# Kernel tuning notes

Hardware: AMD Instinct MI355X
Metric: run time of the kernel (lower is better)

## Reference

```python
import jax, jax.numpy as jnp
import numpy as np

N = 8192      # nodes
DIN = 128     # in_channels
DH = 64       # hidden_channels (dim_out, num_heads=1)
DOUT = 32     # out_channels
RATIO = 0.5
K_KEEP = int(np.ceil(RATIO * N))  # SAGPooling keep count (single graph)
LN_EPS = 1e-5


def _linear_params(k, fan_in, fan_out):
    kw, kb = jax.random.split(k)
    W = jax.random.normal(kw, (fan_in, fan_out), dtype=jnp.float32) / jnp.sqrt(jnp.float32(fan_in))
    b = jax.random.normal(kb, (fan_out,), dtype=jnp.float32) * 0.01
    return W, b


def setup_inputs() -> dict:
    key = jax.random.key(0)
    ks = jax.random.split(key, 8)
    x = jax.random.normal(ks[0], (N, DIN), dtype=jnp.float32)
    batch = jnp.zeros((N,), dtype=jnp.int64)  # single graph
    Wq, bq = _linear_params(ks[1], DIN, DH)
    Wk, bk = _linear_params(ks[2], DIN, DH)
    Wv, bv = _linear_params(ks[3], DIN, DH)
    gcn_W, gcn_b = _linear_params(ks[4], DH, DH)       # GCNConv weight/bias
    score_W, score_b = _linear_params(ks[5], DH, 1)    # SAGPooling score GCNConv
    ln_g = jnp.ones((DH,), dtype=jnp.float32)
    ln_b = jnp.zeros((DH,), dtype=jnp.float32)
    head_W, head_b = _linear_params(ks[6], DH, DOUT)
    return dict(x=x, batch=batch, Wq=Wq, bq=bq, Wk=Wk, bk=bk, Wv=Wv, bv=bv,
                gcn_W=gcn_W, gcn_b=gcn_b, score_W=score_W, score_b=score_b,
                ln_g=ln_g, ln_b=ln_b, head_W=head_W, head_b=head_b)


def _forward(x, Wq, bq, Wk, bk, Wv, bv, gcn_W, gcn_b, score_W, score_b,
             ln_g, ln_b, head_W, head_b):
    # --- self-attention over all nodes (num_heads = 1) ---
    Q = x @ Wq + bq                                        # [N, DH]
    K = x @ Wk + bk
    V = x @ Wv + bv
    attn = jax.nn.softmax(Q @ K.T / jnp.sqrt(jnp.float32(DH)), axis=-1)  # [N, N]
    h = attn @ V                                           # [N, DH]

    # --- edge construction: threshold attention, ensure self-loops ---
    # (attn > 0.5).nonzero() -> edge set; empty -> self-loop fallback; then
    # add_self_loops. Dense equivalent: A = max(mask, I).
    eye = jnp.eye(N, dtype=x.dtype)
    A = jnp.maximum((attn > 0.5).astype(x.dtype), eye)     # [N, N], diag = 1

    # symmetric GCN normalization  D^{-1/2} A D^{-1/2}
    dinv = jax.lax.rsqrt(A.sum(axis=1))                    # [N]
    An = dinv[:, None] * A * dinv[None, :]                 # [N, N]

    # --- GCNConv layer ---
    g = An @ (h @ gcn_W) + gcn_b                           # [N, DH]

    # --- SAGPooling: GCNConv scorer -> tanh -> global top-k (single graph) ---
    score = jnp.tanh((An @ (g @ score_W) + score_b).squeeze(-1))  # [N]
    top_scores, perm = jax.lax.top_k(score, K_KEEP)        # sorted desc, like PyG topk
    xp = g[perm] * top_scores[:, None]                     # [K, DH], multiplier = 1

    # --- LayerNorm + ReLU (dropout is identity in eval) ---
    mu = xp.mean(axis=-1, keepdims=True)
    var = xp.var(axis=-1, keepdims=True)
    xp = (xp - mu) * jax.lax.rsqrt(var + LN_EPS) * ln_g + ln_b
    xp = jax.nn.relu(xp)

    # --- prediction head ---
    return xp @ head_W + head_b                            # [K, DOUT]


def reference(x, batch, Wq, bq, Wk, bk, Wv, bv, gcn_W, gcn_b,
              score_W, score_b, ln_g, ln_b, head_W, head_b):
    del batch  # single graph; grouping has no effect on the math
    return _forward(x, Wq, bq, Wk, bk, Wv, bv, gcn_W, gcn_b,
                    score_W, score_b, ln_g, ln_b, head_W, head_b)
```

## Files before the change

kernel.cpp:

```cpp
#include <hip/hip_runtime.h>
#include <hip/hip_bf16.h>
#include <cstdio>

typedef __hip_bfloat16 bf16;
typedef __attribute__((ext_vector_type(8))) short v8s;
typedef __attribute__((ext_vector_type(4))) short v4s;
typedef __attribute__((ext_vector_type(4))) float v4f;
typedef __attribute__((ext_vector_type(4))) double v4d;

#define MFMA16(a, b, c) __builtin_amdgcn_mfma_f32_16x16x32_bf16((a), (b), (c), 0, 0, 0)

#define NN 8192
#define DIN 128
#define DH 64
#define DOUT 32
#define KKEEP 4096
#define SPLITS 16
#define SPATT 8

__device__ __forceinline__ float bf2f(bf16 v) { return __bfloat162float(v); }
__device__ __forceinline__ short f2bfs(float f) {
  __hip_bfloat16 h = __float2bfloat16(f);
  return *reinterpret_cast<short*>(&h);
}
__device__ __forceinline__ bf16 f2bf(float v) { return __float2bfloat16(v); }

__device__ __forceinline__ double exp_d(double s) {
  const double L2E    = 1.4426950408889634074;
  const double LN2_HI = 6.93147180369123816490e-01;
  const double LN2_LO = 1.90821492927058770002e-10;
  double t  = s * L2E;
  double kf = rint(t);
  double r  = fma(-kf, LN2_HI, s);
  r = fma(-kf, LN2_LO, r);
  double p = 1.0 / 362880.0;
  p = fma(p, r, 1.0 / 40320.0);
  p = fma(p, r, 1.0 / 5040.0);
  p = fma(p, r, 1.0 / 720.0);
  p = fma(p, r, 1.0 / 120.0);
  p = fma(p, r, 1.0 / 24.0);
  p = fma(p, r, 1.0 / 6.0);
  p = fma(p, r, 0.5);
  p = fma(p, r, 1.0);
  p = fma(p, r, 1.0);
  int k = (int)kf;
  long long bits = ((long long)(1023 + k)) << 52;
  double sc = __longlong_as_double(bits);
  return p * sc;
}

__global__ void k0_ucb(const float* __restrict__ gW, const float* __restrict__ sW,
                       const float* __restrict__ gb, double* __restrict__ u) {
  int c = threadIdx.x;
  double acc = 0.0, accb = 0.0;
  for (int d = 0; d < DH; ++d) {
    double swd = (double)sW[d];
    acc  = fma((double)gW[c * DH + d], swd, acc);
    accb = fma((double)gb[d], swd, accb);
  }
  u[c] = acc;
  if (c == 0) u[64] = accb;
}

__global__ __launch_bounds__(256) void k1_prep(
    const float* __restrict__ x, const float* __restrict__ Wq, const float* __restrict__ bq,
    const float* __restrict__ Wk, const float* __restrict__ bk, const float* __restrict__ Wv,
    const float* __restrict__ bv, const double* __restrict__ u,
    double* __restrict__ Qd, double* __restrict__ Kd, double* __restrict__ w,
    bf16* __restrict__ Qb, bf16* __restrict__ Kb, bf16* __restrict__ Vt) {
  __shared__ double xs[16][DIN];
  int t = threadIdx.x;
  int nb = blockIdx.x * 16;
  for (int idx = t; idx < 16 * DIN; idx += 256)
    xs[idx >> 7][idx & 127] = (double)x[(size_t)nb * DIN + idx];
  __syncthreads();
  int d = t & 63;
  int sub = t >> 6;
  double bqd = (double)bq[d];
  double bkd = (double)bk[d];
  double bvd = (double)bv[d];
  double ud = u[d];
  for (int pass = 0; pass < 4; ++pass) {
    int n = pass * 4 + sub;
    double aq = bqd, ak = bkd, av = bvd;
#pragma unroll 8
    for (int c = 0; c < DIN; ++c) {
      double xv = xs[n][c];
      aq = fma(xv, (double)Wq[c * DH + d], aq);
      ak = fma(xv, (double)Wk[c * DH + d], ak);
      av = fma(xv, (double)Wv[c * DH + d], av);
    }
    aq *= 0.125;
    int node = nb + n;
    Qd[(size_t)node * DH + d] = aq;
    Kd[(size_t)node * DH + d] = ak;
    Qb[(size_t)node * DH + d] = f2bf((float)aq);
    Kb[(size_t)node * DH + d] = f2bf((float)ak);
    Vt[(size_t)d * NN + node] = f2bf((float)av);
    double pw = av * ud;
#pragma unroll
    for (int off = 32; off; off >>= 1) pw += __shfl_xor(pw, off);
    if (d == 0) w[node] = pw;
  }
}

__global__ __launch_bounds__(256) void k2_scores(
    const double* __restrict__ Qd, const double* __restrict__ Kd, const double* __restrict__ w,
    double* __restrict__ Zp, double* __restrict__ Wp, double* __restrict__ Ep, int* __restrict__ Jp) {
  __shared__ __align__(16) double Kbuf[2][16][66];
  const int t = threadIdx.x;
  const int wv = t >> 6;
  const int l = t & 63;
  const int li = l & 15, lg = l >> 4;
  const int rb = (blockIdx.x & 127) * 64;
  const int sp = blockIdx.x >> 7;
  const int cbeg = sp * (NN / SPLITS);

  double qreg[16];
  const double* qrow = Qd + (size_t)(rb + 16 * wv + li) * DH + lg;
#pragma unroll
  for (int tt = 0; tt < 16; ++tt) qreg[tt] = qrow[4 * tt];

  {
    const double* src = Kd + (size_t)cbeg * DH;
    int r = t >> 4, c = (t & 15) * 4;
    *(double2*)&Kbuf[0][r][c]     = *(const double2*)&src[r * DH + c];
    *(double2*)&Kbuf[0][r][c + 2] = *(const double2*)&src[r * DH + c + 2];
  }
  __syncthreads();

  double Zt[4] = {0, 0, 0, 0}, Wt[4] = {0, 0, 0, 0}, Et[4] = {-1, -1, -1, -1};
  int Jt[4] = {0, 0, 0, 0};

  const int NT = (NN / SPLITS) / 16;
  for (int kt = 0; kt < NT; ++kt) {
    const int buf = kt & 1;
    if (kt + 1 < NT) {
      const double* src = Kd + (size_t)(cbeg + (kt + 1) * 16) * DH;
      int r = t >> 4, c = (t & 15) * 4;
      *(double2*)&Kbuf[buf ^ 1][r][c]     = *(const double2*)&src[r * DH + c];
      *(double2*)&Kbuf[buf ^ 1][r][c + 2] = *(const double2*)&src[r * DH + c + 2];
    }
    v4d acc = (v4d){0.0, 0.0, 0.0, 0.0};
#pragma unroll
    for (int tt = 0; tt < 16; ++tt) {
      double bfrag = Kbuf[buf][li][4 * tt + lg];
      acc = __builtin_amdgcn_mfma_f64_16x16x4f64(qreg[tt], bfrag, acc, 0, 0, 0);
    }
    const int col = cbeg + kt * 16 + li;
    const double wj = w[col];
#pragma unroll
    for (int v = 0; v < 4; ++v) {
      double e = exp_d(acc[v]);
      Zt[v] += e;
      Wt[v] = fma(e, wj, Wt[v]);
      if (e > Et[v]) { Et[v] = e; Jt[v] = col; }
    }
    __syncthreads();
  }

#pragma unroll
  for (int v = 0; v < 4; ++v) {
#pragma unroll
    for (int m = 1; m < 16; m <<= 1) {
      Zt[v] += __shfl_xor(Zt[v], m);
      Wt[v] += __shfl_xor(Wt[v], m);
      double e2 = __shfl_xor(Et[v], m);
      int j2 = __shfl_xor(Jt[v], m);
      if (e2 > Et[v] || (e2 == Et[v] && j2 < Jt[v])) { Et[v] = e2; Jt[v] = j2; }
    }
  }
  if (li == 0) {
#pragma unroll
    for (int v = 0; v < 4; ++v) {
      int row = rb + 16 * wv + lg + 4 * v;
      Zp[sp * NN + row] = Zt[v];
      Wp[sp * NN + row] = Wt[v];
      Ep[sp * NN + row] = Et[v];
      Jp[sp * NN + row] = Jt[v];
    }
  }
}

__global__ void k3_combine(const double* __restrict__ Zp, const double* __restrict__ Wp,
                           const double* __restrict__ Ep, const int* __restrict__ Jp,
                           double* __restrict__ tau, int* __restrict__ extra, int* __restrict__ jmA) {
  int i = blockIdx.x * 256 + threadIdx.x;
  double Z = 0, W = 0, E = -1;
  int J = 0;
  for (int sp = 0; sp < SPLITS; ++sp) {
    Z += Zp[sp * NN + i];
    W += Wp[sp * NN + i];
    double e = Ep[sp * NN + i];
    if (e > E || (e == E && Jp[sp * NN + i] < J)) { E = e; J = Jp[sp * NN + i]; }
  }
  tau[i] = W / Z;
  extra[i] = (E > 0.5 * Z) && (J != i);
  jmA[i] = J & (NN - 1);
}

__global__ __launch_bounds__(256) void k4_mfma(const bf16* __restrict__ Qb, const bf16* __restrict__ Kb,
                                               const bf16* __restrict__ Vt,
                                               float* __restrict__ hp, float* __restrict__ zp) {
  __shared__ __align__(16) short P[4][16 * 40];
  const int t = threadIdx.x;
  const int wv = t >> 6;
  const int l = t & 63, g = l >> 4, li = l & 15;
  const int qb = (blockIdx.x & 127) * 64 + wv * 16;
  const int sp = blockIdx.x >> 7;
  short* Pw = &P[wv][0];
  const v8s q0 = *(const v8s*)(Qb + (size_t)(qb + li) * DH + g * 8);
  const v8s q1 = *(const v8s*)(Qb + (size_t)(qb + li) * DH + 32 + g * 8);
  v4f hacc[4];
#pragma unroll
  for (int db = 0; db < 4; ++db) hacc[db] = (v4f){0.f, 0.f, 0.f, 0.f};
  float zl = 0.f;
  const int kbeg = sp * (NN / SPATT);
  for (int jb = kbeg; jb < kbeg + NN / SPATT; jb += 32) {
    const bf16* kp = Kb + (size_t)(jb + li) * DH + g * 8;
    v8s ka0 = *(const v8s*)(kp);
    v8s ka1 = *(const v8s*)(kp + 32);
    v8s kb0 = *(const v8s*)(kp + 16 * DH);
    v8s kb1 = *(const v8s*)(kp + 16 * DH + 32);
    v4f c0 = (v4f){0.f, 0.f, 0.f, 0.f}, c1 = (v4f){0.f, 0.f, 0.f, 0.f};
    c0 = MFMA16(ka0, q0, c0);
    c0 = MFMA16(ka1, q1, c0);
    c1 = MFMA16(kb0, q0, c1);
    c1 = MFMA16(kb1, q1, c1);
    v4s p0, p1;
#pragma unroll
    for (int r = 0; r < 4; ++r) {
      short b0 = f2bfs(__expf(c0[r]));
      short b1 = f2bfs(__expf(c1[r]));
      p0[r] = b0;
      p1[r] = b1;
      zl += bf2f(*reinterpret_cast<bf16*>(&b0));
      zl += bf2f(*reinterpret_cast<bf16*>(&b1));
    }
    *(v4s*)&Pw[li * 40 + g * 4] = p0;
    *(v4s*)&Pw[li * 40 + 16 + g * 4] = p1;
    v8s pf = *(const v8s*)&Pw[li * 40 + g * 8];
#pragma unroll
    for (int db = 0; db < 4; ++db) {
      const v8s vb = *(const v8s*)(Vt + (size_t)(db * 16 + li) * NN + jb + g * 8);
      hacc[db] = MFMA16(pf, vb, hacc[db]);
    }
  }
  zl += __shfl_xor(zl, 16);
  zl += __shfl_xor(zl, 32);
  if (g == 0) zp[sp * NN + qb + li] = zl;
#pragma unroll
  for (int r = 0; r < 4; ++r) {
    int row = qb + g * 4 + r;
#pragma unroll
    for (int db = 0; db < 4; ++db)
      hp[((size_t)sp * NN + row) * DH + db * 16 + li] = hacc[db][r];
  }
}

__global__ __launch_bounds__(256) void k9_hM(const float* __restrict__ hp, const float* __restrict__ zp,
                                             const float* __restrict__ gW, float* __restrict__ M) {
  __shared__ float xs[4][DH];
  int t = threadIdx.x;
  int sub = t >> 6, d = t & 63;
  int n = blockIdx.x * 4 + sub;
  float Z = 0.f, H = 0.f;
#pragma unroll
  for (int sp = 0; sp < SPATT; ++sp) {
    Z += zp[sp * NN + n];
    H += hp[((size_t)sp * NN + n) * DH + d];
  }
  xs[sub][d] = H / Z;
  __syncthreads();
  float acc = 0.f;
#pragma unroll 8
  for (int c = 0; c < DH; ++c) acc = fmaf(xs[sub][c], gW[c * DH + d], acc);
  M[(size_t)n * DH + d] = acc;
}

__global__ void k5_t(const double* __restrict__ tau, const int* __restrict__ extra,
                     const int* __restrict__ jmA, const double* __restrict__ u, double* __restrict__ tarr) {
  int i = blockIdx.x * 256 + threadIdx.x;
  int ex = extra[i];
  double di = ex ? 0.70710678118654752440 : 1.0;
  double acc = di * tau[i];
  if (ex) {
    int j = jmA[i] & (NN - 1);
    double dj = extra[j] ? 0.70710678118654752440 : 1.0;
    acc = fma(dj, tau[j], acc);
  }
  tarr[i] = fma(di, acc, u[64]);
}

__global__ void k6_pre(const double* __restrict__ tarr, const int* __restrict__ extra,
                       const int* __restrict__ jmA, const float* __restrict__ score_b,
                       double* __restrict__ pre, float* __restrict__ sc32, int* __restrict__ cnt) {
  int i = blockIdx.x * 256 + threadIdx.x;
  int ex = extra[i];
  double di = ex ? 0.70710678118654752440 : 1.0;
  double acc = di * tarr[i];
  if (ex) {
    int j = jmA[i] & (NN - 1);
    double dj = extra[j] ? 0.70710678118654752440 : 1.0;
    acc = fma(dj, tarr[j], acc);
  }
  double p = fma(di, acc, (double)score_b[0]);
  pre[i] = p;
  sc32[i] = (float)tanh(p);
  cnt[i] = 0;
}

__global__ void k7_rank(const double* __restrict__ pre, int* __restrict__ cnt) {
  __shared__ double pj[512];
  int i = (blockIdx.x & 31) * 256 + threadIdx.x;
  int j0 = (blockIdx.x >> 5) * 512;
  for (int k = threadIdx.x; k < 512; k += 256) pj[k] = pre[j0 + k];
  __syncthreads();
  double si = pre[i];
  int c = 0;
#pragma unroll 8
  for (int j = 0; j < 512; ++j) {
    double v = pj[j];
    c += (v > si || (v == si && (j0 + j) < i));
  }
  atomicAdd(&cnt[i], c);
}

__global__ void k8_sel(const int* __restrict__ cnt, int* __restrict__ sel) {
  int i = blockIdx.x * 256 + threadIdx.x;
  unsigned r = (unsigned)cnt[i];
  if (r < KKEEP) sel[r] = i;
}

__global__ __launch_bounds__(256) void k11_head(const float* __restrict__ M, const int* __restrict__ extra,
                                                const int* __restrict__ jmA, const float* __restrict__ gb,
                                                const float* __restrict__ sc32, const int* __restrict__ sel,
                                                const float* __restrict__ lg, const float* __restrict__ lb,
                                                const float* __restrict__ hW, const float* __restrict__ hb,
                                                float* __restrict__ out) {
  __shared__ float xs[4][DH];
  int t = threadIdx.x;
  int wv = t >> 6, d = t & 63;
  int p = blockIdx.x * 4 + wv;
  int i = sel[p] & (NN - 1);
  int ex = extra[i];
  float di = ex ? 0.70710678f : 1.0f;
  float acc0 = di * M[(size_t)i * DH + d];
  if (ex) {
    int j = jmA[i] & (NN - 1);
    acc0 = fmaf(extra[j] ? 0.70710678f : 1.0f, M[(size_t)j * DH + d], acc0);
  }
  float gval = fmaf(di, acc0, gb[d]);
  float v = gval * sc32[i];
  float s1 = v;
#pragma unroll
  for (int off = 32; off; off >>= 1) s1 += __shfl_xor(s1, off);
  float mu = s1 * (1.0f / 64.0f);
  float dv = v - mu;
  float s2 = dv * dv;
#pragma unroll
  for (int off = 32; off; off >>= 1) s2 += __shfl_xor(s2, off);
  float var = s2 * (1.0f / 64.0f);
  float xn = dv * rsqrtf(var + 1e-5f) * lg[d] + lb[d];
  xs[wv][d] = fmaxf(xn, 0.0f);
  __syncthreads();
  if (t < 128) {
    int r = t >> 5, o = t & 31;
    float acc = hb[o];
#pragma unroll 8
    for (int c = 0; c < DH; ++c) acc = fmaf(xs[r][c], hW[c * DOUT + o], acc);
    out[(size_t)(blockIdx.x * 4 + r) * DOUT + o] = acc;
  }
}

#define MB 1048576ull
constexpr size_t OFF_QD   = 0 * MB;
constexpr size_t OFF_KD   = 4 * MB;
constexpr size_t OFF_M    = 16 * MB;
constexpr size_t OFF_ZP   = 20 * MB;
constexpr size_t OFF_WP   = 21 * MB;
constexpr size_t OFF_EP   = 22 * MB;
constexpr size_t OFF_JP   = 23 * MB;
constexpr size_t OFF_W    = 24 * MB;
constexpr size_t OFF_U    = 25 * MB;
constexpr size_t OFF_TAU  = 26 * MB;
constexpr size_t OFF_EX   = 27 * MB;
constexpr size_t OFF_JM   = 28 * MB;
constexpr size_t OFF_T    = 29 * MB;
constexpr size_t OFF_PRE  = 30 * MB;
constexpr size_t OFF_SC   = 31 * MB;
constexpr size_t OFF_CNT  = 32 * MB;
constexpr size_t OFF_SEL  = 33 * MB;
constexpr size_t OFF_HP   = 34 * MB;
constexpr size_t OFF_ZATT = 50 * MB;
constexpr size_t OFF_QB   = 51 * MB;
constexpr size_t OFF_KB   = 52 * MB;
constexpr size_t OFF_VT   = 53 * MB;
constexpr size_t WS_NEEDED = 54 * MB;

extern "C" void kernel_launch(void* const* d_in, const int* in_sizes, int n_in,
                              void* d_out, int out_size, void* d_ws, size_t ws_size,
                              hipStream_t stream) {
  if (n_in < 16 || ws_size < WS_NEEDED || out_size != KKEEP * DOUT) {
    fprintf(stderr, "[sag] GUARD ws=%zu need=%zu n_in=%d out=%d\n", ws_size, WS_NEEDED, n_in, out_size);
    return;
  }
  const float* x   = (const float*)d_in[0];
  const float* Wq  = (const float*)d_in[2];
  const float* bq  = (const float*)d_in[3];
  const float* Wk  = (const float*)d_in[4];
  const float* bk  = (const float*)d_in[5];
  const float* Wv  = (const float*)d_in[6];
  const float* bv  = (const float*)d_in[7];
  const float* gW  = (const float*)d_in[8];
  const float* gb  = (const float*)d_in[9];
  const float* sW  = (const float*)d_in[10];
  const float* sb  = (const float*)d_in[11];
  const float* lg  = (const float*)d_in[12];
  const float* lb  = (const float*)d_in[13];
  const float* hW  = (const float*)d_in[14];
  const float* hb  = (const float*)d_in[15];
  float* out = (float*)d_out;

  char* ws = (char*)d_ws;
  double* Qd  = (double*)(ws + OFF_QD);
  double* Kd  = (double*)(ws + OFF_KD);
  bf16*   Qb  = (bf16*)(ws + OFF_QB);
  bf16*   Kb  = (bf16*)(ws + OFF_KB);
  bf16*   Vt  = (bf16*)(ws + OFF_VT);
  float*  M   = (float*)(ws + OFF_M);
  double* Zp  = (double*)(ws + OFF_ZP);
  double* Wp  = (double*)(ws + OFF_WP);
  double* Ep  = (double*)(ws + OFF_EP);
  int*    Jp  = (int*)(ws + OFF_JP);
  double* w   = (double*)(ws + OFF_W);
  double* u   = (double*)(ws + OFF_U);
  double* tau = (double*)(ws + OFF_TAU);
  int*    ex  = (int*)(ws + OFF_EX);
  int*    jm  = (int*)(ws + OFF_JM);
  double* tarr= (double*)(ws + OFF_T);
  double* pre = (double*)(ws + OFF_PRE);
  float*  sc32= (float*)(ws + OFF_SC);
  int*    cnt = (int*)(ws + OFF_CNT);
  int*    sel = (int*)(ws + OFF_SEL);
  float*  hp  = (float*)(ws + OFF_HP);
  float*  zatt= (float*)(ws + OFF_ZATT);

  hipLaunchKernelGGL(k0_ucb, dim3(1), dim3(64), 0, stream, gW, sW, gb, u);
  hipLaunchKernelGGL(k1_prep, dim3(512), dim3(256), 0, stream, x, Wq, bq, Wk, bk, Wv, bv, u,
                     Qd, Kd, w, Qb, Kb, Vt);
  hipLaunchKernelGGL(k2_scores, dim3(128 * SPLITS), dim3(256), 0, stream, Qd, Kd, w, Zp, Wp, Ep, Jp);
  hipLaunchKernelGGL(k3_combine, dim3(32), dim3(256), 0, stream, Zp, Wp, Ep, Jp, tau, ex, jm);
  hipLaunchKernelGGL(k4_mfma, dim3(128 * SPATT), dim3(256), 0, stream, Qb, Kb, Vt, hp, zatt);
  hipLaunchKernelGGL(k9_hM, dim3(2048), dim3(256), 0, stream, hp, zatt, gW, M);
  hipLaunchKernelGGL(k5_t, dim3(32), dim3(256), 0, stream, tau, ex, jm, u, tarr);
  hipLaunchKernelGGL(k6_pre, dim3(32), dim3(256), 0, stream, tarr, ex, jm, sb, pre, sc32, cnt);
  hipLaunchKernelGGL(k7_rank, dim3(512), dim3(256), 0, stream, pre, cnt);
  hipLaunchKernelGGL(k8_sel, dim3(32), dim3(256), 0, stream, cnt, sel);
  hipLaunchKernelGGL(k11_head, dim3(1024), dim3(256), 0, stream, M, ex, jm, gb, sc32, sel,
                     lg, lb, hW, hb, out);
}
```

Measured before the change: 405.6 us.

## Fuse combine and two-hop propagation kernels, fold u computation into prep

Removes the tiny k0 kernel by having each k1_prep thread compute its own u entry inline, and merges k3_combine, k5_t and k6_pre into one kernel k356 that recomputes the split reductions for neighbours on demand instead of passing tau and tarr through global buffers. This cuts four launches and the dependencies between them. In exchange, each node may re-reduce the 16 split partials for up to four neighbour nodes, giving redundant gather reads, and every thread recomputes the 64-term bias dot product.

```diff
diff --git a/kernel.cpp b/kernel.cpp
--- a/kernel.cpp
+++ b/kernel.cpp
@@ -17,6 +17,7 @@
 #define KKEEP 4096
 #define SPLITS 16
 #define SPATT 8
+#define RS2 0.70710678118654752440
 
 __device__ __forceinline__ float bf2f(bf16 v) { return __bfloat162float(v); }
 __device__ __forceinline__ short f2bfs(float f) {
@@ -49,23 +50,10 @@
   return p * sc;
 }
 
-__global__ void k0_ucb(const float* __restrict__ gW, const float* __restrict__ sW,
-                       const float* __restrict__ gb, double* __restrict__ u) {
-  int c = threadIdx.x;
-  double acc = 0.0, accb = 0.0;
-  for (int d = 0; d < DH; ++d) {
-    double swd = (double)sW[d];
-    acc  = fma((double)gW[c * DH + d], swd, acc);
-    accb = fma((double)gb[d], swd, accb);
-  }
-  u[c] = acc;
-  if (c == 0) u[64] = accb;
-}
-
 __global__ __launch_bounds__(256) void k1_prep(
     const float* __restrict__ x, const float* __restrict__ Wq, const float* __restrict__ bq,
     const float* __restrict__ Wk, const float* __restrict__ bk, const float* __restrict__ Wv,
-    const float* __restrict__ bv, const double* __restrict__ u,
+    const float* __restrict__ bv, const float* __restrict__ gW, const float* __restrict__ sW,
     double* __restrict__ Qd, double* __restrict__ Kd, double* __restrict__ w,
     bf16* __restrict__ Qb, bf16* __restrict__ Kb, bf16* __restrict__ Vt) {
   __shared__ double xs[16][DIN];
@@ -76,10 +64,11 @@
   __syncthreads();
   int d = t & 63;
   int sub = t >> 6;
+  double ud = 0.0;
+  for (int dd = 0; dd < DH; ++dd) ud = fma((double)gW[d * DH + dd], (double)sW[dd], ud);
   double bqd = (double)bq[d];
   double bkd = (double)bk[d];
   double bvd = (double)bv[d];
-  double ud = u[d];
   for (int pass = 0; pass < 4; ++pass) {
     int n = pass * 4 + sub;
     double aq = bqd, ak = bkd, av = bvd;
@@ -182,21 +171,67 @@
   }
 }
 
-__global__ void k3_combine(const double* __restrict__ Zp, const double* __restrict__ Wp,
-                           const double* __restrict__ Ep, const int* __restrict__ Jp,
-                           double* __restrict__ tau, int* __restrict__ extra, int* __restrict__ jmA) {
-  int i = blockIdx.x * 256 + threadIdx.x;
-  double Z = 0, W = 0, E = -1;
+__device__ __forceinline__ double tau_of(int k, const double* __restrict__ Zp,
+                                         const double* __restrict__ Wp) {
+  double Z = 0, W = 0;
+  for (int sp = 0; sp < SPLITS; ++sp) { Z += Zp[sp * NN + k]; W += Wp[sp * NN + k]; }
+  return W / Z;
+}
+__device__ __forceinline__ void exj_of(int k, const double* __restrict__ Zp,
+                                       const double* __restrict__ Ep, const int* __restrict__ Jp,
+                                       int& exo, int& jo) {
+  double Z = 0, E = -1;
   int J = 0;
   for (int sp = 0; sp < SPLITS; ++sp) {
-    Z += Zp[sp * NN + i];
-    W += Wp[sp * NN + i];
-    double e = Ep[sp * NN + i];
-    if (e > E || (e == E && Jp[sp * NN + i] < J)) { E = e; J = Jp[sp * NN + i]; }
-  }
-  tau[i] = W / Z;
-  extra[i] = (E > 0.5 * Z) && (J != i);
-  jmA[i] = J & (NN - 1);
+    Z += Zp[sp * NN + k];
+    double e = Ep[sp * NN + k];
+    if (e > E || (e == E && Jp[sp * NN + k] < J)) { E = e; J = Jp[sp * NN + k]; }
+  }
+  exo = (E > 0.5 * Z) && (J != k);
+  jo = J & (NN - 1);
+}
+__device__ __forceinline__ double tarr_of(int k, const double* __restrict__ Zp,
+                                          const double* __restrict__ Wp,
+                                          const double* __restrict__ Ep,
+                                          const int* __restrict__ Jp, double cb) {
+  int exk, jk;
+  exj_of(k, Zp, Ep, Jp, exk, jk);
+  double dk = exk ? RS2 : 1.0;
+  double acc = dk * tau_of(k, Zp, Wp);
+  if (exk) {
+    int exj, jj;
+    exj_of(jk, Zp, Ep, Jp, exj, jj);
+    double dj = exj ? RS2 : 1.0;
+    acc = fma(dj, tau_of(jk, Zp, Wp), acc);
+  }
+  return fma(dk, acc, cb);
+}
+
+__global__ void k356(const double* __restrict__ Zp, const double* __restrict__ Wp,
+                     const double* __restrict__ Ep, const int* __restrict__ Jp,
+                     const float* __restrict__ gb, const float* __restrict__ sW,
+                     const float* __restrict__ score_b,
+                     int* __restrict__ ex_out, int* __restrict__ jm_out,
+                     double* __restrict__ pre, float* __restrict__ sc32, int* __restrict__ cnt) {
+  int i = blockIdx.x * 256 + threadIdx.x;
+  double cb = 0.0;
+  for (int d = 0; d < DH; ++d) cb = fma((double)gb[d], (double)sW[d], cb);
+  int exi, ji;
+  exj_of(i, Zp, Ep, Jp, exi, ji);
+  ex_out[i] = exi;
+  jm_out[i] = ji;
+  double di = exi ? RS2 : 1.0;
+  double acc = di * tarr_of(i, Zp, Wp, Ep, Jp, cb);
+  if (exi) {
+    int exj, jj;
+    exj_of(ji, Zp, Ep, Jp, exj, jj);
+    double dj = exj ? RS2 : 1.0;
+    acc = fma(dj, tarr_of(ji, Zp, Wp, Ep, Jp, cb), acc);
+  }
+  double p = fma(di, acc, (double)score_b[0]);
+  pre[i] = p;
+  sc32[i] = (float)tanh(p);
+  cnt[i] = 0;
 }
 
 __global__ __launch_bounds__(256) void k4_mfma(const bf16* __restrict__ Qb, const bf16* __restrict__ Kb,
@@ -276,38 +311,6 @@
 #pragma unroll 8
   for (int c = 0; c < DH; ++c) acc = fmaf(xs[sub][c], gW[c * DH + d], acc);
   M[(size_t)n * DH + d] = acc;
-}
-
-__global__ void k5_t(const double* __restrict__ tau, const int* __restrict__ extra,
-                     const int* __restrict__ jmA, const double* __restrict__ u, double* __restrict__ tarr) {
-  int i = blockIdx.x * 256 + threadIdx.x;
-  int ex = extra[i];
-  double di = ex ? 0.70710678118654752440 : 1.0;
-  double acc = di * tau[i];
-  if (ex) {
-    int j = jmA[i] & (NN - 1);
-    double dj = extra[j] ? 0.70710678118654752440 : 1.0;
-    acc = fma(dj, tau[j], acc);
-  }
-  tarr[i] = fma(di, acc, u[64]);
-}
-
-__global__ void k6_pre(const double* __restrict__ tarr, const int* __restrict__ extra,
-                       const int* __restrict__ jmA, const float* __restrict__ score_b,
-                       double* __restrict__ pre, float* __restrict__ sc32, int* __restrict__ cnt) {
-  int i = blockIdx.x * 256 + threadIdx.x;
-  int ex = extra[i];
-  double di = ex ? 0.70710678118654752440 : 1.0;
-  double acc = di * tarr[i];
-  if (ex) {
-    int j = jmA[i] & (NN - 1);
-    double dj = extra[j] ? 0.70710678118654752440 : 1.0;
-    acc = fma(dj, tarr[j], acc);
-  }
-  double p = fma(di, acc, (double)score_b[0]);
-  pre[i] = p;
-  sc32[i] = (float)tanh(p);
-  cnt[i] = 0;
 }
 
 __global__ void k7_rank(const double* __restrict__ pre, int* __restrict__ cnt) {
@@ -382,11 +385,8 @@
 constexpr size_t OFF_EP   = 22 * MB;
 constexpr size_t OFF_JP   = 23 * MB;
 constexpr size_t OFF_W    = 24 * MB;
-constexpr size_t OFF_U    = 25 * MB;
-constexpr size_t OFF_TAU  = 26 * MB;
 constexpr size_t OFF_EX   = 27 * MB;
 constexpr size_t OFF_JM   = 28 * MB;
-constexpr size_t OFF_T    = 29 * MB;
 constexpr size_t OFF_PRE  = 30 * MB;
 constexpr size_t OFF_SC   = 31 * MB;
 constexpr size_t OFF_CNT  = 32 * MB;
@@ -434,11 +434,8 @@
   double* Ep  = (double*)(ws + OFF_EP);
   int*    Jp  = (int*)(ws + OFF_JP);
   double* w   = (double*)(ws + OFF_W);
-  double* u   = (double*)(ws + OFF_U);
-  double* tau = (double*)(ws + OFF_TAU);
   int*    ex  = (int*)(ws + OFF_EX);
   int*    jm  = (int*)(ws + OFF_JM);
-  double* tarr= (double*)(ws + OFF_T);
   double* pre = (double*)(ws + OFF_PRE);
   float*  sc32= (float*)(ws + OFF_SC);
   int*    cnt = (int*)(ws + OFF_CNT);
@@ -446,15 +443,13 @@
   float*  hp  = (float*)(ws + OFF_HP);
   float*  zatt= (float*)(ws + OFF_ZATT);
 
-  hipLaunchKernelGGL(k0_ucb, dim3(1), dim3(64), 0, stream, gW, sW, gb, u);
-  hipLaunchKernelGGL(k1_prep, dim3(512), dim3(256), 0, stream, x, Wq, bq, Wk, bk, Wv, bv, u,
-                     Qd, Kd, w, Qb, Kb, Vt);
+  hipLaunchKernelGGL(k1_prep, dim3(512), dim3(256), 0, stream, x, Wq, bq, Wk, bk, Wv, bv,
+                     gW, sW, Qd, Kd, w, Qb, Kb, Vt);
   hipLaunchKernelGGL(k2_scores, dim3(128 * SPLITS), dim3(256), 0, stream, Qd, Kd, w, Zp, Wp, Ep, Jp);
-  hipLaunchKernelGGL(k3_combine, dim3(32), dim3(256), 0, stream, Zp, Wp, Ep, Jp, tau, ex, jm);
   hipLaunchKernelGGL(k4_mfma, dim3(128 * SPATT), dim3(256), 0, stream, Qb, Kb, Vt, hp, zatt);
   hipLaunchKernelGGL(k9_hM, dim3(2048), dim3(256), 0, stream, hp, zatt, gW, M);
-  hipLaunchKernelGGL(k5_t, dim3(32), dim3(256), 0, stream, tau, ex, jm, u, tarr);
-  hipLaunchKernelGGL(k6_pre, dim3(32), dim3(256), 0, stream, tarr, ex, jm, sb, pre, sc32, cnt);
+  hipLaunchKernelGGL(k356, dim3(32), dim3(256), 0, stream, Zp, Wp, Ep, Jp, gb, sW, sb,
+                     ex, jm, pre, sc32, cnt);
   hipLaunchKernelGGL(k7_rank, dim3(512), dim3(256), 0, stream, pre, cnt);
   hipLaunchKernelGGL(k8_sel, dim3(32), dim3(256), 0, stream, cnt, sel);
   hipLaunchKernelGGL(k11_head, dim3(1024), dim3(256), 0, stream, M, ex, jm, gb, sc32, sel,
```

Result: no change. 402.1 us (-0.9%).
